# Kernel optimization log

Hardware: AMD Instinct MI355X
Metric: run time of the kernel (lower is better)

Reference implementation:

```python
import jax, jax.numpy as jnp
import numpy as np

IMG_SIZE = 224
ALPHA = 100.0  # hardcoded softmax temperature in knnsearch_t_grad


def _sqdist(a, b):
    # (B,N,C),(B,M,C) -> (B,N,M) squared euclidean distances
    return (jnp.sum(a * a, -1)[:, :, None]
            - 2.0 * jnp.einsum('bnc,bmc->bnm', a, b)
            + jnp.sum(b * b, -1)[:, None, :])


def _cdist(a, b):
    return jnp.sqrt(jnp.maximum(_sqdist(a, b), 1e-12))


def proj2img(pc, img_offset):
    # faithful jax port of GraphDeformLoss_Neural_Partial.proj2img
    B, N, _ = pc.shape
    pc_max = pc.max(axis=1)              # (B,3)
    pc_min_full = pc.min(axis=1)         # (B,3)
    pc_range = pc_max - pc_min_full
    grid_size = pc_range[:, :2].max(axis=-1) / (IMG_SIZE - 3)   # (B,)
    pc_min = pc_min_full[:, None, :2]                            # (B,1,2)
    gs = grid_size[:, None, None]
    idx_xy = jnp.floor((pc[:, :, :2] - pc_min) / gs)             # (B,N,2)
    # densify each point into a 5x5 neighborhood of pixels
    idx_dense = (idx_xy[:, :, None, :] + img_offset[None, None]).reshape(B, N * 25, 2) + 1.0
    center = jnp.floor((idx_dense.max(axis=1) + idx_dense.min(axis=1)) / 2.0)  # (B,2)
    offset = IMG_SIZE / 2.0 - center - 1.0                       # (B,2) = (offset_x, offset_y)
    idx_off = idx_dense + offset[:, None, :]
    # boundary correction as in the torch code, plus clip for safety
    idx_off = idx_off + (idx_off < 0).astype(jnp.float32) - (idx_off > IMG_SIZE - 1).astype(jnp.float32)
    idx_off = jnp.clip(idx_off, 0, IMG_SIZE - 1)
    f_dense = jnp.repeat(jnp.repeat(pc[:, :, None, 2:3], 25, axis=2).reshape(B, N * 25, 1), 3, axis=-1)
    flat = (idx_off[..., 0] * IMG_SIZE + idx_off[..., 1]).astype(jnp.int32)   # (B,N*25)
    out = jax.vmap(lambda f, i: jax.ops.segment_sum(f, i, num_segments=IMG_SIZE * IMG_SIZE))(f_dense, flat)
    img = out.reshape(B, IMG_SIZE, IMG_SIZE, 3).transpose(0, 3, 1, 2)  # (B,3,H,W)
    return jax.nn.sigmoid(img)


def setup_inputs() -> dict:
    key = jax.random.key(0)
    k1, k2, k3, k4 = jax.random.split(key, 4)
    B, N, M, C = 4, 4995, 4995, 128
    off = jnp.array([[i, j] for i in range(-2, 3) for j in range(-2, 3)], dtype=jnp.float32)
    return {
        'verts1': jax.random.normal(k1, (B, N, 3), jnp.float32),
        'verts2': jax.random.normal(k2, (B, M, 3), jnp.float32),
        'feat1': jax.random.normal(k3, (B, N, C), jnp.float32),
        'feat2': jax.random.normal(k4, (B, M, C), jnp.float32),
        'img_offset': off,
        'k': 10,
    }


def reference(verts1, verts2, feat1, feat2, img_offset, k):
    # knnsearch_t_grad: soft correspondence from feature-space cdist + softmax
    d_feat = _cdist(feat1, feat2)                               # (B,N,M)
    Pi_12 = jax.nn.softmax(-ALPHA * d_feat, axis=-1)
    verts12 = jnp.einsum('bnm,bmc->bnc', Pi_12, verts2)         # pulled-back points (B,N,3)
    # chamfer (squared distances, as chamfer_3DDist); partial: take dist1 branch (N<=M)
    d2 = _sqdist(verts12, verts2)
    self_rec_loss = jnp.mean(jnp.min(d2, axis=-1))
    # knn_grad + index_points: gather k-NN features on source cloud
    d2_11 = _sqdist(verts1, verts1)
    _, idx11 = jax.lax.top_k(-d2_11, k)                         # (B,N,k) nearest
    feat1_conv = jax.vmap(lambda p, i: p[i])(feat1, idx11)      # (B,N,k,C)
    deform_feat_loss = jnp.mean((feat1_conv - feat1[:, :, None, :]) ** 2)
    # point-to-image projection loss
    img1 = proj2img(verts12, img_offset)
    img2 = proj2img(verts2, img_offset)
    img_loss = jnp.mean((img1 - img2) ** 2)
    return self_rec_loss + img_loss + deform_feat_loss
```

## Files before the change

### kernel.cpp

```cpp
#include <hip/hip_runtime.h>
#include <math.h>

#define BB 4
#define NN 4995
#define CC 128
#define IMG 224
#define IMGP (IMG*IMG)
#define ALPHA_F 100.0f
#define SPLITS 8
#define COLS_PER_SPLIT 640
#define RBLK 40
#define NG 158
#define NCP 5120
#define NTAP (2*BB*NN*25)
#define NREP 4
#define TKCAP 256

#define SM_SCALE 20813.6898f
#define NEG2S   -41627.3796f
#define EPS_S    2.08136898e-8f

#define OFF_V12    0
#define OFF_FN1    60000
#define OFF_V1Q    81000
#define OFF_V2Q    161000
#define OFF_C2Q    241000
#define OFF_PART   323000
#define OFF_IMG1   1123000
#define OFF_IMG2   1323704
#define OFF_ACC    1524408
#define OFF_STATS  1524792
#define OFF_F2H    1525000
#define OFF_F2L    2820000
#define OFF_IMGR   4115000
#define WS_NEED_REP ((size_t)5721000*sizeof(float))
#define ZERO_START OFF_IMG1
#define ZERO_FLOATS (1524920 - OFF_IMG1)

typedef short v8s  __attribute__((ext_vector_type(8)));
typedef float v16f __attribute__((ext_vector_type(16)));

#if __has_builtin(__builtin_amdgcn_exp2f)
__device__ __forceinline__ float fast_exp2(float x){ return __builtin_amdgcn_exp2f(x); }
#else
__device__ __forceinline__ float fast_exp2(float x){ float r; asm("v_exp_f32 %0, %1" : "=v"(r) : "v"(x)); return r; }
#endif
#if __has_builtin(__builtin_amdgcn_sqrtf)
__device__ __forceinline__ float fast_sqrt(float x){ return __builtin_amdgcn_sqrtf(x); }
#else
__device__ __forceinline__ float fast_sqrt(float x){ float r; asm("v_sqrt_f32 %0, %1" : "=v"(r) : "v"(x)); return r; }
#endif

__device__ __forceinline__ float wave_min(float v){
#pragma unroll
  for (int off=32; off; off>>=1) v = fminf(v, __shfl_xor(v, off));
  return v;
}
__device__ __forceinline__ float wave_sum(float v){
#pragma unroll
  for (int off=32; off; off>>=1) v += __shfl_xor(v, off);
  return v;
}

__device__ __forceinline__ int pack_bf_hi(float a, float b){
  return (int)__builtin_amdgcn_perm(__float_as_uint(b), __float_as_uint(a), 0x07060302u);
}

__device__ __forceinline__ void cvt_hilo(float4 a, float4 c, int4& hi, int4& lo){
  float hx=__uint_as_float(__float_as_uint(a.x)&0xffff0000u);
  float hy=__uint_as_float(__float_as_uint(a.y)&0xffff0000u);
  float hz=__uint_as_float(__float_as_uint(a.z)&0xffff0000u);
  float hw=__uint_as_float(__float_as_uint(a.w)&0xffff0000u);
  float gx=__uint_as_float(__float_as_uint(c.x)&0xffff0000u);
  float gy=__uint_as_float(__float_as_uint(c.y)&0xffff0000u);
  float gz=__uint_as_float(__float_as_uint(c.z)&0xffff0000u);
  float gw=__uint_as_float(__float_as_uint(c.w)&0xffff0000u);
  hi = make_int4(pack_bf_hi(a.x,a.y), pack_bf_hi(a.z,a.w),
                 pack_bf_hi(c.x,c.y), pack_bf_hi(c.z,c.w));
  lo = make_int4(pack_bf_hi(a.x-hx,a.y-hy), pack_bf_hi(a.z-hz,a.w-hw),
                 pack_bf_hi(c.x-gx,c.y-gy), pack_bf_hi(c.z-gz,c.w-gw));
}

__device__ __forceinline__ v8s i4_to_s8(int4 v){
  union { int4 i; v8s s; } u; u.i = v; return u.s;
}

__device__ __forceinline__ void gld_lds16(const void* g, void* l){
  __builtin_amdgcn_global_load_lds((const __attribute__((address_space(1))) void*)g,
                                   (__attribute__((address_space(3))) void*)l, 16, 0, 0);
}

__device__ __forceinline__ unsigned int fkey(float f){
  unsigned int u = __float_as_uint(f);
  return ((int)u < 0) ? ~u : (u ^ 0x80000000u);
}

__global__ __launch_bounds__(256) void k_norms(const float* __restrict__ verts1, const float* __restrict__ verts2,
                        const float* __restrict__ feat1, float* __restrict__ ws) {
  int gt = blockIdx.x*blockDim.x + threadIdx.x;
  int i = gt >> 2, sub = gt & 3;
  if (i >= BB*NCP) return;
  int b = i / NCP, col = i - b*NCP;
  if (col >= NN){
    if (sub == 0)
      ((float4*)(ws+OFF_C2Q))[i] = make_float4(0.f,0.f,0.f,1e30f);
    return;
  }
  int r = b*NN + col;
  const float4* fa = (const float4*)(feat1 + (size_t)r*CC) + sub*8;
  float s1=0.f;
#pragma unroll
  for (int k=0;k<8;k++){
    float4 t = fa[k];
    s1 = fmaf(t.x,t.x,s1); s1 = fmaf(t.y,t.y,s1); s1 = fmaf(t.z,t.z,s1); s1 = fmaf(t.w,t.w,s1);
  }
  s1 += __shfl_xor(s1,1); s1 += __shfl_xor(s1,2);
  if (sub == 0){
    float x=verts1[(size_t)r*3], y=verts1[(size_t)r*3+1], z=verts1[(size_t)r*3+2];
    ((float4*)(ws+OFF_V1Q))[r] = make_float4(x,y,z, x*x+y*y+z*z);
    float x2=verts2[(size_t)r*3], y2=verts2[(size_t)r*3+1], z2=verts2[(size_t)r*3+2];
    ((float4*)(ws+OFF_V2Q))[r] = make_float4(x2,y2,z2, x2*x2+y2*y2+z2*z2);
    ws[OFF_FN1+r] = SM_SCALE*s1;
  }
}

__global__ __launch_bounds__(256) void k_conv(const float* __restrict__ feat2,
                                              const float* __restrict__ verts2,
                                              float* __restrict__ ws) {
  __shared__ float s2p[8][32];
  int g = blockIdx.x, b = blockIdx.y;
  int t = threadIdx.x;
  int q = t >> 5, c32 = t & 31;
  int col = g*32 + c32; if (col > NN-1) col = NN-1;
  const float4* src = (const float4*)(feat2 + ((size_t)(b*NN + col))*CC) + q*4;
  float4 v0 = src[0], v1 = src[1], v2 = src[2], v3 = src[3];
  {
    float s2 = 0.f;
    s2=fmaf(v0.x,v0.x,s2); s2=fmaf(v0.y,v0.y,s2); s2=fmaf(v0.z,v0.z,s2); s2=fmaf(v0.w,v0.w,s2);
    s2=fmaf(v1.x,v1.x,s2); s2=fmaf(v1.y,v1.y,s2); s2=fmaf(v1.z,v1.z,s2); s2=fmaf(v1.w,v1.w,s2);
    s2=fmaf(v2.x,v2.x,s2); s2=fmaf(v2.y,v2.y,s2); s2=fmaf(v2.z,v2.z,s2); s2=fmaf(v2.w,v2.w,s2);
    s2=fmaf(v3.x,v3.x,s2); s2=fmaf(v3.y,v3.y,s2); s2=fmaf(v3.z,v3.z,s2); s2=fmaf(v3.w,v3.w,s2);
    s2p[q][c32] = s2;
  }
  short* f2h = (short*)(ws + OFF_F2H);
  short* f2l = (short*)(ws + OFF_F2L);
  size_t base = ((size_t)(b*NG + g))*4096 + (size_t)q*512 + c32*8;
  int4 hi, lo;
  cvt_hilo(v0, v1, hi, lo);
  *(int4*)&f2h[base] = hi;  *(int4*)&f2l[base] = lo;
  cvt_hilo(v2, v3, hi, lo);
  *(int4*)&f2h[base + 256] = hi;  *(int4*)&f2l[base + 256] = lo;
  __syncthreads();
  if (t < 32){
    int c = g*32 + t;
    if (c < NN){
      float S2 = ((s2p[0][t]+s2p[1][t])+(s2p[2][t]+s2p[3][t]))
               + ((s2p[4][t]+s2p[5][t])+(s2p[6][t]+s2p[7][t]));
      size_t r = (size_t)(b*NN + c);
      float x2=verts2[r*3], y2=verts2[r*3+1], z2=verts2[r*3+2];
      ((float4*)(ws+OFF_C2Q))[(size_t)b*NCP + c] = make_float4(x2,y2,z2, SM_SCALE*S2);
    }
  }
}

__global__ __launch_bounds__(256) void k_stageA(const float* __restrict__ feat1,
      float* __restrict__ ws) {
  __shared__ __align__(16) short Bbuf[2][4096];
  __shared__ __align__(16) float colq[768*4];

  int rblk  = blockIdx.x;
  int split = blockIdx.y;
  int b     = blockIdx.z;
  int rowBase = rblk*128;
  int colBase = split*COLS_PER_SPLIT;
  int colEnd  = colBase + COLS_PER_SPLIT; if (colEnd > NN) colEnd = NN;
  int nct = (colEnd - colBase + 63) >> 6;
  int nst = nct << 2;

  int t    = threadIdx.x;
  int w    = t >> 6;
  int lane = t & 63;
  int half = lane >> 5;
  int m32  = lane & 31;

  const float* f1b = feat1 + (size_t)b*NN*CC;
  const short* f2h = (const short*)(ws + OFF_F2H);
  const short* f2l = (const short*)(ws + OFF_F2L);
  const float4* cqb = (const float4*)(ws + OFF_C2Q) + (size_t)b*NCP;

#pragma unroll
  for (int r=0; r<3; r++){
    int col = colBase + r*256 + t; if (col > NCP-1) col = NCP-1;
    gld_lds16(cqb + col, &colq[(r*256 + w*64)*4]);
  }

  size_t f2base = (((size_t)(b*NG) + (colBase>>5) + (w>>1)) << 12) + (size_t)((t&127)*8);

  {
    short* d = &Bbuf[0][0] + w*512;
    gld_lds16(f2h + f2base, d);
    gld_lds16(f2l + f2base, d + 2048);
  }

  int nrow = rowBase + w*32 + m32;
  int nclamp = nrow > NN-1 ? NN-1 : nrow;
  float sn = ws[OFF_FN1 + (size_t)b*NN + nclamp];
  const float4* ar = (const float4*)(f1b + (size_t)nclamp*CC) + (half<<1);
  v8s Afh[8], Afl[8];
#pragma unroll
  for (int sl=0; sl<8; ++sl){
    float4 v0 = ar[sl*4], v1 = ar[sl*4+1];
    int4 hi, lo;
    cvt_hilo(v0, v1, hi, lo);
    Afh[sl] = i4_to_s8(hi); Afl[sl] = i4_to_s8(lo);
  }

  __syncthreads();

  float mm = INFINITY, S = 0.f, Vx = 0.f, Vy = 0.f, Vz = 0.f;

  for (int ci = 0; ci < nct; ci++){
    v16f acc0, acc1;
#pragma unroll
    for (int i=0;i<16;i++){ acc0[i]=0.f; acc1[i]=0.f; }

#pragma unroll
    for (int kt = 0; kt < 4; kt++){
      int s = (ci<<2) + kt;
      if (s+1 < nst){
        int s1 = s+1;
        size_t so = f2base + ((size_t)(s1>>2)<<13) + ((size_t)(s1&3)<<10);
        short* d = &Bbuf[0][0] + ((s1&1)<<12) + w*512;
        gld_lds16(f2h + so, d);
        gld_lds16(f2l + so, d + 2048);
      }
      const short* Bh = &Bbuf[0][0] + ((s&1)<<12);
      const short* Bl = Bh + 2048;
#pragma unroll
      for (int kh=0; kh<2; kh++){
        int fo = (kh<<9) + (half<<8) + (m32<<3);
        v8s a0h = *(const v8s*)&Bh[fo];
        v8s a0l = *(const v8s*)&Bl[fo];
        v8s a1h = *(const v8s*)&Bh[1024+fo];
        v8s a1l = *(const v8s*)&Bl[1024+fo];
        v8s b1h = Afh[kt*2+kh];
        v8s b1l = Afl[kt*2+kh];
        __builtin_amdgcn_s_setprio(1);
        acc0 = __builtin_amdgcn_mfma_f32_32x32x16_bf16(a0h, b1h, acc0, 0,0,0);
        acc0 = __builtin_amdgcn_mfma_f32_32x32x16_bf16(a0h, b1l, acc0, 0,0,0);
        acc0 = __builtin_amdgcn_mfma_f32_32x32x16_bf16(a0l, b1h, acc0, 0,0,0);
        acc1 = __builtin_amdgcn_mfma_f32_32x32x16_bf16(a1h, b1h, acc1, 0,0,0);
        acc1 = __builtin_amdgcn_mfma_f32_32x32x16_bf16(a1h, b1l, acc1, 0,0,0);
        acc1 = __builtin_amdgcn_mfma_f32_32x32x16_bf16(a1l, b1h, acc1, 0,0,0);
        __builtin_amdgcn_s_setprio(0);
      }
      __syncthreads();
    }

    int cb4 = ci<<8;
    float Mt = INFINITY;
#pragma unroll
    for (int reg=0; reg<16; reg++){
      int cp0 = (reg&3) + 8*(reg>>2) + 4*half;
      float f0 = colq[cb4 + cp0*4 + 3];
      float d0 = fmaf(NEG2S, acc0[reg], sn) + f0;
      float p0 = fast_sqrt(fmaxf(d0, EPS_S));
      acc0[reg] = p0; Mt = fminf(Mt, p0);
      float f1v = colq[cb4 + (cp0+32)*4 + 3];
      float d1 = fmaf(NEG2S, acc1[reg], sn) + f1v;
      float p1 = fast_sqrt(fmaxf(d1, EPS_S));
      acc1[reg] = p1; Mt = fminf(Mt, p1);
    }
    float mn = fminf(mm, Mt);
    float sc = fast_exp2(mn - mm);
    float se=0.f, sx=0.f, sy=0.f, sz=0.f;
#pragma unroll
    for (int reg=0; reg<16; reg++){
      int cp0 = (reg&3) + 8*(reg>>2) + 4*half;
      float4 q0 = *(const float4*)&colq[cb4 + cp0*4];
      float e0 = fast_exp2(mn - acc0[reg]);
      se += e0; sx=fmaf(e0,q0.x,sx); sy=fmaf(e0,q0.y,sy); sz=fmaf(e0,q0.z,sz);
      float4 q1 = *(const float4*)&colq[cb4 + (cp0+32)*4];
      float e1 = fast_exp2(mn - acc1[reg]);
      se += e1; sx=fmaf(e1,q1.x,sx); sy=fmaf(e1,q1.y,sy); sz=fmaf(e1,q1.z,sz);
    }
    S  = fmaf(S,  sc, se);
    Vx = fmaf(Vx, sc, sx);
    Vy = fmaf(Vy, sc, sy);
    Vz = fmaf(Vz, sc, sz);
    mm = mn;
  }

  {
    float m2  = __shfl_xor(mm, 32);
    float S2  = __shfl_xor(S,  32);
    float Vx2 = __shfl_xor(Vx, 32);
    float Vy2 = __shfl_xor(Vy, 32);
    float Vz2 = __shfl_xor(Vz, 32);
    float M = fminf(mm, m2);
    float c1 = fast_exp2(M - mm), c2 = fast_exp2(M - m2);
    float Sf  = S*c1  + S2*c2;
    float Vxf = Vx*c1 + Vx2*c2;
    float Vyf = Vy*c1 + Vy2*c2;
    float Vzf = Vz*c1 + Vz2*c2;
    if (half==0 && nrow < NN){
      float* p = ws + OFF_PART + ((size_t)(b*NN+nrow)*SPLITS + split)*5;
      p[0]=M; p[1]=Sf; p[2]=Vxf; p[3]=Vyf; p[4]=Vzf;
    }
  }
}

__global__ void k_combine(float* __restrict__ ws) {
  int row = blockIdx.x*blockDim.x + threadIdx.x;
  if (row >= BB*NN) return;
  const float* p = ws + OFF_PART + (size_t)row*SPLITS*5;
  float mm = INFINITY;
#pragma unroll
  for (int s=0;s<SPLITS;s++) mm = fminf(mm, p[s*5]);
  float S=0.f,Vx=0.f,Vy=0.f,Vz=0.f;
#pragma unroll
  for (int s=0;s<SPLITS;s++){
    float sc = fast_exp2(mm - p[s*5]);
    S  += p[s*5+1]*sc; Vx += p[s*5+2]*sc; Vy += p[s*5+3]*sc; Vz += p[s*5+4]*sc;
  }
  ws[OFF_V12+(size_t)row*3+0]=Vx/S;
  ws[OFF_V12+(size_t)row*3+1]=Vy/S;
  ws[OFF_V12+(size_t)row*3+2]=Vz/S;
}

__global__ __launch_bounds__(256) void k_selfrec(float* __restrict__ ws) {
  int rblk = blockIdx.x, b = blockIdx.y;
  int lane = threadIdx.x & 63, w = threadIdx.x >> 6;
  int r0 = rblk*32 + w*8;
  const float4* v2q = (const float4*)(ws + OFF_V2Q) + (size_t)b*NN;
  const float* v12 = ws + OFF_V12 + (size_t)b*NN*3;
  float xr[8], yr[8], zr[8], sar[8]; bool val[8];
#pragma unroll
  for (int j=0;j<8;j++){
    int n = r0+j; val[j] = (n < NN); int nc = val[j] ? n : NN-1;
    float x=v12[(size_t)nc*3], y=v12[(size_t)nc*3+1], z=v12[(size_t)nc*3+2];
    sar[j]=x*x+y*y+z*z;
    xr[j]=-2.0f*x; yr[j]=-2.0f*y; zr[j]=-2.0f*z;
  }
  float mn[8];
#pragma unroll
  for (int j=0;j<8;j++) mn[j] = INFINITY;
  for (int m=lane; m<NN; m+=64) {
    float4 q = v2q[m];
#pragma unroll
    for (int j=0;j<8;j++)
      mn[j] = fminf(mn[j], fmaf(xr[j],q.x, fmaf(yr[j],q.y, fmaf(zr[j],q.z, q.w))));
  }
  float s = 0.f;
#pragma unroll
  for (int j=0;j<8;j++){
    float v = wave_min(mn[j]);
    s += val[j] ? (v + sar[j]) : 0.f;
  }
  if (lane==0)
    atomicAdd(((double*)(ws+OFF_ACC)) + ((rblk*4 + w) & 63), (double)s);
}

__global__ __launch_bounds__(256) void k_topk(const float* __restrict__ feat1,
        const int* __restrict__ kptr, float* __restrict__ ws) {
  __shared__ unsigned int keybuf[4*256];
  __shared__ unsigned long long cand[4*TKCAP];
  __shared__ int scnt[4];
  __shared__ float tfs[4];
  __shared__ int sel[4][16];
  __shared__ float rs[4];
  int t = threadIdx.x;
  int lane = t & 63, wid = t >> 6;
  int b = blockIdx.y;
  int n0 = blockIdx.x*4;
  int kk = *kptr; if (kk > 16) kk = 16; if (kk < 1) kk = 1;

  const float4* v1q = (const float4*)(ws + OFF_V1Q) + (size_t)b*NN;
  float mx[4], my2[4], mz[4];
#pragma unroll
  for (int j=0;j<4;j++){
    int n = n0+j; if (n > NN-1) n = NN-1;
    float4 me = v1q[n];
    mx[j]=-2.0f*me.x; my2[j]=-2.0f*me.y; mz[j]=-2.0f*me.z;
  }
  if (t < 4) scnt[t] = 0;

  float mn[4] = {INFINITY, INFINITY, INFINITY, INFINITY};
  for (int i=0;i<20;i++){
    int m = t + 256*i;
    if (m < NN){
      float4 q = v1q[m];
#pragma unroll
      for (int j=0;j<4;j++){
        float d = fmaf(mx[j], q.x, fmaf(my2[j], q.y, fmaf(mz[j], q.z, q.w)));
        mn[j] = fminf(mn[j], d);
      }
    }
  }

#pragma unroll
  for (int j=0;j<4;j++)
    keybuf[j*256 + t] = fkey(mn[j]) >> 16;
  __syncthreads();

  {
    unsigned int k0 = keybuf[wid*256 + lane];
    unsigned int k1 = keybuf[wid*256 + 64 + lane];
    unsigned int k2 = keybuf[wid*256 + 128 + lane];
    unsigned int k3 = keybuf[wid*256 + 192 + lane];
    unsigned int prefix = 0;
    for (int bit=15; bit>=0; --bit){
      unsigned int piv = prefix | (1u<<bit);
      int c = __popcll(__ballot(k0 < piv)) + __popcll(__ballot(k1 < piv))
            + __popcll(__ballot(k2 < piv)) + __popcll(__ballot(k3 < piv));
      if (c < kk) prefix = piv;
    }
    unsigned int K = (prefix<<16) | 0xFFFFu;
    unsigned int fb = (K & 0x80000000u) ? (K ^ 0x80000000u) : ~K;
    if (lane==0) tfs[wid] = __uint_as_float(fb);
  }
  __syncthreads();
  float tf0 = tfs[0], tf1 = tfs[1], tf2 = tfs[2], tf3 = tfs[3];

  bool g0 = (mn[0] <= tf0), g1 = (mn[1] <= tf1), g2 = (mn[2] <= tf2), g3 = (mn[3] <= tf3);
  if (g0|g1|g2|g3){
    for (int i=0;i<20;i++){
      int m = t + 256*i;
      if (m < NN){
        float4 q = v1q[m];
        float sw = q.w;
        float d0 = fmaf(mx[0], q.x, fmaf(my2[0], q.y, fmaf(mz[0], q.z, sw)));
        float d1 = fmaf(mx[1], q.x, fmaf(my2[1], q.y, fmaf(mz[1], q.z, sw)));
        float d2 = fmaf(mx[2], q.x, fmaf(my2[2], q.y, fmaf(mz[2], q.z, sw)));
        float d3 = fmaf(mx[3], q.x, fmaf(my2[3], q.y, fmaf(mz[3], q.z, sw)));
        if (g0 && d0 <= tf0){
          int pos = atomicAdd(&scnt[0], 1);
          if (pos < TKCAP) cand[0*TKCAP + pos] = ((unsigned long long)fkey(d0) << 13) | (unsigned int)m;
        }
        if (g1 && d1 <= tf1){
          int pos = atomicAdd(&scnt[1], 1);
          if (pos < TKCAP) cand[1*TKCAP + pos] = ((unsigned long long)fkey(d1) << 13) | (unsigned int)m;
        }
        if (g2 && d2 <= tf2){
          int pos = atomicAdd(&scnt[2], 1);
          if (pos < TKCAP) cand[2*TKCAP + pos] = ((unsigned long long)fkey(d2) << 13) | (unsigned int)m;
        }
        if (g3 && d3 <= tf3){
          int pos = atomicAdd(&scnt[3], 1);
          if (pos < TKCAP) cand[3*TKCAP + pos] = ((unsigned long long)fkey(d3) << 13) | (unsigned int)m;
        }
      }
    }
  }
  __syncthreads();

  {
    int cnt = scnt[wid]; if (cnt > TKCAP) cnt = TKCAP;
    unsigned long long kv0 = (lane       < cnt) ? cand[wid*TKCAP + lane]       : ~0ull;
    unsigned long long kv1 = (lane + 64  < cnt) ? cand[wid*TKCAP + lane + 64]  : ~0ull;
    unsigned long long kv2 = (lane + 128 < cnt) ? cand[wid*TKCAP + lane + 128] : ~0ull;
    unsigned long long kv3 = (lane + 192 < cnt) ? cand[wid*TKCAP + lane + 192] : ~0ull;
    int r0=0, r1=0, r2=0, r3=0;
    for (int q2=0; q2<cnt; ++q2){
      unsigned long long cj = cand[wid*TKCAP + q2];
      r0 += (cj < kv0); r1 += (cj < kv1); r2 += (cj < kv2); r3 += (cj < kv3);
    }
    if (lane       < cnt && r0 < kk) sel[wid][r0] = (int)(kv0 & 8191ull);
    if (lane + 64  < cnt && r1 < kk) sel[wid][r1] = (int)(kv1 & 8191ull);
    if (lane + 128 < cnt && r2 < kk) sel[wid][r2] = (int)(kv2 & 8191ull);
    if (lane + 192 < cnt && r3 < kk) sel[wid][r3] = (int)(kv3 & 8191ull);
  }
  __syncthreads();

  float mse = 0.f;
  int c = t & 127;
  int rh = t >> 7;
  for (int j=0;j<4;j++){
    int n = n0+j;
    if (n >= NN) break;
    const float* f1n = feat1 + ((size_t)b*NN + n)*CC;
    float e = f1n[c];
    for (int r=rh; r<kk; r+=2){
      const float* g = feat1 + ((size_t)b*NN + sel[j][r])*CC;
      float d = g[c]-e;
      mse = fmaf(d,d,mse);
    }
  }

  float acc = wave_sum(mse);
  if (lane==0) rs[wid] = acc;
  __syncthreads();
  if (t==0){
    float s = (rs[0]+rs[1])+(rs[2]+rs[3]);
    atomicAdd(((double*)(ws+OFF_ACC)) + 128 + ((blockIdx.x + b) & 63), (double)s);
  }
}

__global__ void k_imgstats(const float* __restrict__ verts2, const float* __restrict__ imgoff,
                           float* __restrict__ ws) {
  __shared__ float r0[4], r1[4], r2[4], r3[4];
  __shared__ float sgs, smnx, smny;
  int img = blockIdx.x >> 2, b = blockIdx.x & 3;
  const float* pc = (img==0) ? (ws + OFF_V12 + (size_t)b*NN*3) : (verts2 + (size_t)b*NN*3);
  int lane = threadIdx.x & 63, wid = threadIdx.x >> 6;
  float mnx=INFINITY, mxx=-INFINITY, mny=INFINITY, mxy=-INFINITY;
  for (int n = threadIdx.x; n < NN; n += 256) {
    float x = pc[(size_t)n*3], y = pc[(size_t)n*3+1];
    mnx=fminf(mnx,x); mxx=fmaxf(mxx,x); mny=fminf(mny,y); mxy=fmaxf(mxy,y);
  }
#pragma unroll
  for (int off=32; off; off>>=1) {
    mnx=fminf(mnx,__shfl_xor(mnx,off)); mxx=fmaxf(mxx,__shfl_xor(mxx,off));
    mny=fminf(mny,__shfl_xor(mny,off)); mxy=fmaxf(mxy,__shfl_xor(mxy,off));
  }
  if (lane==0){ r0[wid]=mnx; r1[wid]=mxx; r2[wid]=mny; r3[wid]=mxy; }
  __syncthreads();
  float* st = ws + OFF_STATS + (size_t)(img*4+b)*16;
  if (threadIdx.x==0){
    mnx=fminf(fminf(r0[0],r0[1]),fminf(r0[2],r0[3]));
    mxx=fmaxf(fmaxf(r1[0],r1[1]),fmaxf(r1[2],r1[3]));
    mny=fminf(fminf(r2[0],r2[1]),fminf(r2[2],r2[3]));
    mxy=fmaxf(fmaxf(r3[0],r3[1]),fmaxf(r3[2],r3[3]));
    float gs = fmaxf(mxx-mnx, mxy-mny) / 221.0f;
    sgs=gs; smnx=mnx; smny=mny;
    st[0]=mnx; st[1]=mxx; st[2]=mny; st[3]=mxy; st[4]=gs;
  }
  __syncthreads();
  float gs=sgs, bx=smnx, by=smny;
  float fmnx=INFINITY, fmxx=-INFINITY, fmny=INFINITY, fmxy=-INFINITY;
  for (int n = threadIdx.x; n < NN; n += 256) {
    float fx = floorf((pc[(size_t)n*3]-bx)/gs);
    float fy = floorf((pc[(size_t)n*3+1]-by)/gs);
    fmnx=fminf(fmnx,fx); fmxx=fmaxf(fmxx,fx); fmny=fminf(fmny,fy); fmxy=fmaxf(fmxy,fy);
  }
#pragma unroll
  for (int off=32; off; off>>=1) {
    fmnx=fminf(fmnx,__shfl_xor(fmnx,off)); fmxx=fmaxf(fmxx,__shfl_xor(fmxx,off));
    fmny=fminf(fmny,__shfl_xor(fmny,off)); fmxy=fmaxf(fmxy,__shfl_xor(fmxy,off));
  }
  __syncthreads();
  if (lane==0){ r0[wid]=fmnx; r1[wid]=fmxx; r2[wid]=fmny; r3[wid]=fmxy; }
  __syncthreads();
  if (threadIdx.x==0){
    fmnx=fminf(fminf(r0[0],r0[1]),fminf(r0[2],r0[3]));
    fmxx=fmaxf(fmaxf(r1[0],r1[1]),fmaxf(r1[2],r1[3]));
    fmny=fminf(fminf(r2[0],r2[1]),fminf(r2[2],r2[3]));
    fmxy=fmaxf(fmaxf(r3[0],r3[1]),fmaxf(r3[2],r3[3]));
    float omnx=INFINITY, omxx=-INFINITY, omny=INFINITY, omxy=-INFINITY;
    for (int l=0;l<25;l++){
      float ox=imgoff[l*2], oy=imgoff[l*2+1];
      omnx=fminf(omnx,ox); omxx=fmaxf(omxx,ox); omny=fminf(omny,oy); omxy=fmaxf(omxy,oy);
    }
    float cx = floorf(((fmxx+omxx+1.0f)+(fmnx+omnx+1.0f))*0.5f);
    float cy = floorf(((fmxy+omxy+1.0f)+(fmny+omny+1.0f))*0.5f);
    st[5] = (112.0f - cx) - 1.0f;
    st[6] = (112.0f - cy) - 1.0f;
  }
}

__global__ __launch_bounds__(256) void k_scatter(const float* __restrict__ verts2,
                          const float* __restrict__ imgoff,
                          float* __restrict__ ws, int nrep) {
  int g = blockIdx.x*256 + threadIdx.x;
  if (g >= NTAP) return;
  int p = g / 25; int l = g - p*25;
  int img = p / (BB*NN); int r = p - img*(BB*NN); int b = r / NN;
  const float* pc = (img==0) ? (ws + OFF_V12) : verts2;
  float x = pc[(size_t)r*3], y = pc[(size_t)r*3+1], z = pc[(size_t)r*3+2];
  const float* st = ws + OFF_STATS + (size_t)(img*4+b)*16;
  float mnx=st[0], mny=st[2], gs=st[4], offx=st[5], offy=st[6];
  float bx = floorf((x-mnx)/gs) + 1.0f + offx;
  float by = floorf((y-mny)/gs) + 1.0f + offy;
  float vx = bx + imgoff[l*2], vy = by + imgoff[l*2+1];
  vx += (vx<0.f?1.f:0.f) - (vx>223.f?1.f:0.f);
  vy += (vy<0.f?1.f:0.f) - (vy>223.f?1.f:0.f);
  vx = fminf(fmaxf(vx,0.f),223.f); vy = fminf(fmaxf(vy,0.f),223.f);
  int flat = (int)(vx*224.f + vy);
  float* im;
  if (nrep > 1)
    im = ws + OFF_IMGR + ((size_t)(((blockIdx.x & (nrep-1))*2 + img)*BB + b))*IMGP;
  else
    im = ws + (img==0?OFF_IMG1:OFF_IMG2) + (size_t)b*IMGP;
  atomicAdd(im + flat, z);
}

__global__ void k_imgloss(float* __restrict__ ws, int nrep) {
  int i = blockIdx.x*blockDim.x + threadIdx.x;
  float v = 0.f;
  if (i < BB*IMGP) {
    float a, c;
    if (nrep > 1){
      a = 0.f; c = 0.f;
      for (int r=0; r<nrep; ++r){
        a += ws[OFF_IMGR + (size_t)(r*2+0)*BB*IMGP + i];
        c += ws[OFF_IMGR + (size_t)(r*2+1)*BB*IMGP + i];
      }
    } else {
      a = ws[OFF_IMG1+i]; c = ws[OFF_IMG2+i];
    }
    float sa = 1.f/(1.f+expf(-a)), sc = 1.f/(1.f+expf(-c));
    float d = sa - sc; v = d*d;
  }
  v = wave_sum(v);
  if ((threadIdx.x&63)==0)
    atomicAdd(((double*)(ws+OFF_ACC)) + 64 + (blockIdx.x & 63), (double)v);
}

__global__ void k_final(const int* __restrict__ kptr, const float* __restrict__ ws, float* __restrict__ out) {
  const double* acc = (const double*)(ws+OFF_ACC);
  int t = threadIdx.x;
  double a0 = acc[t], a1 = acc[64+t], a2 = acc[128+t];
#pragma unroll
  for (int off=32; off; off>>=1){
    a0 += __shfl_down(a0, off);
    a1 += __shfl_down(a1, off);
    a2 += __shfl_down(a2, off);
  }
  if (t==0){
    int kk = *kptr; if (kk > 16) kk = 16; if (kk < 1) kk = 1;
    double srl = a0 / (double)(BB*NN);
    double img = a1 / ((double)BB*IMGP);
    double df  = a2 / ((double)BB*NN*kk*CC);
    out[0] = (float)(srl + img + df);
  }
}

extern "C" void kernel_launch(void* const* d_in, const int* in_sizes, int n_in,
                              void* d_out, int out_size, void* d_ws, size_t ws_size,
                              hipStream_t stream) {
  (void)in_sizes; (void)n_in; (void)out_size;
  const float* verts1 = (const float*)d_in[0];
  const float* verts2 = (const float*)d_in[1];
  const float* feat1  = (const float*)d_in[2];
  const float* feat2  = (const float*)d_in[3];
  const float* imgoff = (const float*)d_in[4];
  const int*   kptr   = (const int*)d_in[5];
  float* ws  = (float*)d_ws;
  float* out = (float*)d_out;
  int nrep = (ws_size >= WS_NEED_REP) ? NREP : 1;

  hipMemsetAsync(ws + ZERO_START, 0, (size_t)ZERO_FLOATS*sizeof(float), stream);
  if (nrep > 1)
    hipMemsetAsync(ws + OFF_IMGR, 0, (size_t)NREP*2*BB*IMGP*sizeof(float), stream);

  k_norms<<<(BB*NCP*4+255)/256, 256, 0, stream>>>(verts1, verts2, feat1, ws);

  dim3 gC(NG, BB);
  k_conv<<<gC, 256, 0, stream>>>(feat2, verts2, ws);

  dim3 gA(RBLK, SPLITS, BB);
  k_stageA<<<gA, 256, 0, stream>>>(feat1, ws);
  k_combine<<<(BB*NN+255)/256, 256, 0, stream>>>(ws);

  dim3 gS((NN+31)/32, BB);
  k_selfrec<<<gS, 256, 0, stream>>>(ws);

  dim3 gT((NN+3)/4, BB);
  k_topk<<<gT, 256, 0, stream>>>(feat1, kptr, ws);

  k_imgstats<<<8, 256, 0, stream>>>(verts2, imgoff, ws);
  k_scatter<<<(NTAP+255)/256, 256, 0, stream>>>(verts2, imgoff, ws, nrep);
  k_imgloss<<<(BB*IMGP+255)/256, 256, 0, stream>>>(ws, nrep);

  k_final<<<1,64,0,stream>>>(kptr, ws, out);
}
```

Before: 343.1 us.

## Fuse norm/convert kernels, persistent stageA with atomic work queue, merge combine into selfrec

```diff
diff --git a/kernel.cpp b/kernel.cpp
--- a/kernel.cpp
+++ b/kernel.cpp
@@ -11,10 +11,13 @@
 #define COLS_PER_SPLIT 640
 #define RBLK 40
 #define NG 158
+#define NGP 160
 #define NCP 5120
 #define NTAP (2*BB*NN*25)
 #define NREP 4
 #define TKCAP 256
+#define NITEMS (RBLK*SPLITS*BB)
+#define GRID_A 1024
 
 #define SM_SCALE 20813.6898f
 #define NEG2S   -41627.3796f
@@ -30,12 +33,14 @@
 #define OFF_IMG2   1323704
 #define OFF_ACC    1524408
 #define OFF_STATS  1524792
+#define OFF_WORK   1524920
 #define OFF_F2H    1525000
 #define OFF_F2L    2820000
 #define OFF_IMGR   4115000
 #define WS_NEED_REP ((size_t)5721000*sizeof(float))
 #define ZERO_START OFF_IMG1
-#define ZERO_FLOATS (1524920 - OFF_IMG1)
+#define ZERO_FLOATS (1524924 - OFF_IMG1)
+#define ZERO2_FLOATS (1524924 - OFF_ACC)
 
 typedef short v8s  __attribute__((ext_vector_type(8)));
 typedef float v16f __attribute__((ext_vector_type(16)));
@@ -95,41 +100,22 @@
   return ((int)u < 0) ? ~u : (u ^ 0x80000000u);
 }
 
-__global__ __launch_bounds__(256) void k_norms(const float* __restrict__ verts1, const float* __restrict__ verts2,
-                        const float* __restrict__ feat1, float* __restrict__ ws) {
-  int gt = blockIdx.x*blockDim.x + threadIdx.x;
-  int i = gt >> 2, sub = gt & 3;
-  if (i >= BB*NCP) return;
-  int b = i / NCP, col = i - b*NCP;
-  if (col >= NN){
-    if (sub == 0)
-      ((float4*)(ws+OFF_C2Q))[i] = make_float4(0.f,0.f,0.f,1e30f);
-    return;
-  }
-  int r = b*NN + col;
-  const float4* fa = (const float4*)(feat1 + (size_t)r*CC) + sub*8;
-  float s1=0.f;
-#pragma unroll
-  for (int k=0;k<8;k++){
-    float4 t = fa[k];
-    s1 = fmaf(t.x,t.x,s1); s1 = fmaf(t.y,t.y,s1); s1 = fmaf(t.z,t.z,s1); s1 = fmaf(t.w,t.w,s1);
-  }
-  s1 += __shfl_xor(s1,1); s1 += __shfl_xor(s1,2);
-  if (sub == 0){
-    float x=verts1[(size_t)r*3], y=verts1[(size_t)r*3+1], z=verts1[(size_t)r*3+2];
-    ((float4*)(ws+OFF_V1Q))[r] = make_float4(x,y,z, x*x+y*y+z*z);
-    float x2=verts2[(size_t)r*3], y2=verts2[(size_t)r*3+1], z2=verts2[(size_t)r*3+2];
-    ((float4*)(ws+OFF_V2Q))[r] = make_float4(x2,y2,z2, x2*x2+y2*y2+z2*z2);
-    ws[OFF_FN1+r] = SM_SCALE*s1;
-  }
-}
-
-__global__ __launch_bounds__(256) void k_conv(const float* __restrict__ feat2,
+__global__ __launch_bounds__(256) void k_conv(const float* __restrict__ feat1,
+                                              const float* __restrict__ feat2,
+                                              const float* __restrict__ verts1,
                                               const float* __restrict__ verts2,
                                               float* __restrict__ ws) {
-  __shared__ float s2p[8][32];
+  __shared__ float s2p[8][32], s1p[8][32];
   int g = blockIdx.x, b = blockIdx.y;
   int t = threadIdx.x;
+  if (g >= NG){
+    if (t < 32){
+      int c = g*32 + t;
+      if (c < NCP)
+        ((float4*)(ws+OFF_C2Q))[(size_t)b*NCP + c] = make_float4(0.f,0.f,0.f,1e30f);
+    }
+    return;
+  }
   int q = t >> 5, c32 = t & 31;
   int col = g*32 + c32; if (col > NN-1) col = NN-1;
   const float4* src = (const float4*)(feat2 + ((size_t)(b*NN + col))*CC) + q*4;
@@ -142,6 +128,16 @@
     s2=fmaf(v3.x,v3.x,s2); s2=fmaf(v3.y,v3.y,s2); s2=fmaf(v3.z,v3.z,s2); s2=fmaf(v3.w,v3.w,s2);
     s2p[q][c32] = s2;
   }
+  {
+    const float4* fa = (const float4*)(feat1 + ((size_t)(b*NN + col))*CC) + q*4;
+    float4 u0 = fa[0], u1 = fa[1], u2 = fa[2], u3 = fa[3];
+    float s1 = 0.f;
+    s1=fmaf(u0.x,u0.x,s1); s1=fmaf(u0.y,u0.y,s1); s1=fmaf(u0.z,u0.z,s1); s1=fmaf(u0.w,u0.w,s1);
+    s1=fmaf(u1.x,u1.x,s1); s1=fmaf(u1.y,u1.y,s1); s1=fmaf(u1.z,u1.z,s1); s1=fmaf(u1.w,u1.w,s1);
+    s1=fmaf(u2.x,u2.x,s1); s1=fmaf(u2.y,u2.y,s1); s1=fmaf(u2.z,u2.z,s1); s1=fmaf(u2.w,u2.w,s1);
+    s1=fmaf(u3.x,u3.x,s1); s1=fmaf(u3.y,u3.y,s1); s1=fmaf(u3.z,u3.z,s1); s1=fmaf(u3.w,u3.w,s1);
+    s1p[q][c32] = s1;
+  }
   short* f2h = (short*)(ws + OFF_F2H);
   short* f2l = (short*)(ws + OFF_F2L);
   size_t base = ((size_t)(b*NG + g))*4096 + (size_t)q*512 + c32*8;
@@ -156,26 +152,26 @@
     if (c < NN){
       float S2 = ((s2p[0][t]+s2p[1][t])+(s2p[2][t]+s2p[3][t]))
                + ((s2p[4][t]+s2p[5][t])+(s2p[6][t]+s2p[7][t]));
+      float S1 = ((s1p[0][t]+s1p[1][t])+(s1p[2][t]+s1p[3][t]))
+               + ((s1p[4][t]+s1p[5][t])+(s1p[6][t]+s1p[7][t]));
       size_t r = (size_t)(b*NN + c);
+      float x=verts1[r*3], y=verts1[r*3+1], z=verts1[r*3+2];
+      ((float4*)(ws+OFF_V1Q))[r] = make_float4(x,y,z, x*x+y*y+z*z);
       float x2=verts2[r*3], y2=verts2[r*3+1], z2=verts2[r*3+2];
+      ((float4*)(ws+OFF_V2Q))[r] = make_float4(x2,y2,z2, x2*x2+y2*y2+z2*z2);
       ((float4*)(ws+OFF_C2Q))[(size_t)b*NCP + c] = make_float4(x2,y2,z2, SM_SCALE*S2);
-    }
-  }
-}
-
-__global__ __launch_bounds__(256) void k_stageA(const float* __restrict__ feat1,
+      ws[OFF_FN1+r] = SM_SCALE*S1;
+    } else if (c < NCP){
+      ((float4*)(ws+OFF_C2Q))[(size_t)b*NCP + c] = make_float4(0.f,0.f,0.f,1e30f);
+    }
+  }
+}
+
+__global__ __launch_bounds__(256, 4) void k_stageA(const float* __restrict__ feat1,
       float* __restrict__ ws) {
   __shared__ __align__(16) short Bbuf[2][4096];
   __shared__ __align__(16) float colq[768*4];
-
-  int rblk  = blockIdx.x;
-  int split = blockIdx.y;
-  int b     = blockIdx.z;
-  int rowBase = rblk*128;
-  int colBase = split*COLS_PER_SPLIT;
-  int colEnd  = colBase + COLS_PER_SPLIT; if (colEnd > NN) colEnd = NN;
-  int nct = (colEnd - colBase + 63) >> 6;
-  int nst = nct << 2;
+  __shared__ int sWi;
 
   int t    = threadIdx.x;
   int w    = t >> 6;
@@ -183,162 +179,192 @@
   int half = lane >> 5;
   int m32  = lane & 31;
 
-  const float* f1b = feat1 + (size_t)b*NN*CC;
-  const short* f2h = (const short*)(ws + OFF_F2H);
-  const short* f2l = (const short*)(ws + OFF_F2L);
-  const float4* cqb = (const float4*)(ws + OFF_C2Q) + (size_t)b*NCP;
-
-#pragma unroll
-  for (int r=0; r<3; r++){
-    int col = colBase + r*256 + t; if (col > NCP-1) col = NCP-1;
-    gld_lds16(cqb + col, &colq[(r*256 + w*64)*4]);
-  }
-
-  size_t f2base = (((size_t)(b*NG) + (colBase>>5) + (w>>1)) << 12) + (size_t)((t&127)*8);
-
-  {
-    short* d = &Bbuf[0][0] + w*512;
-    gld_lds16(f2h + f2base, d);
-    gld_lds16(f2l + f2base, d + 2048);
-  }
-
-  int nrow = rowBase + w*32 + m32;
-  int nclamp = nrow > NN-1 ? NN-1 : nrow;
-  float sn = ws[OFF_FN1 + (size_t)b*NN + nclamp];
-  const float4* ar = (const float4*)(f1b + (size_t)nclamp*CC) + (half<<1);
-  v8s Afh[8], Afl[8];
-#pragma unroll
-  for (int sl=0; sl<8; ++sl){
-    float4 v0 = ar[sl*4], v1 = ar[sl*4+1];
-    int4 hi, lo;
-    cvt_hilo(v0, v1, hi, lo);
-    Afh[sl] = i4_to_s8(hi); Afl[sl] = i4_to_s8(lo);
-  }
-
-  __syncthreads();
-
-  float mm = INFINITY, S = 0.f, Vx = 0.f, Vy = 0.f, Vz = 0.f;
-
-  for (int ci = 0; ci < nct; ci++){
-    v16f acc0, acc1;
-#pragma unroll
-    for (int i=0;i<16;i++){ acc0[i]=0.f; acc1[i]=0.f; }
-
-#pragma unroll
-    for (int kt = 0; kt < 4; kt++){
-      int s = (ci<<2) + kt;
-      if (s+1 < nst){
-        int s1 = s+1;
-        size_t so = f2base + ((size_t)(s1>>2)<<13) + ((size_t)(s1&3)<<10);
-        short* d = &Bbuf[0][0] + ((s1&1)<<12) + w*512;
-        gld_lds16(f2h + so, d);
-        gld_lds16(f2l + so, d + 2048);
+  int* wcnt = (int*)(ws + OFF_WORK);
+  if (t == 0) sWi = atomicAdd(wcnt, 1);
+  __syncthreads();
+
+  while (sWi < NITEMS) {
+    int wi = sWi;
+    int rblk  = wi % RBLK;
+    int qd    = wi / RBLK;
+    int split = qd & 7;
+    int b     = qd >> 3;
+    int rowBase = rblk*128;
+    int colBase = split*COLS_PER_SPLIT;
+    int colEnd  = colBase + COLS_PER_SPLIT; if (colEnd > NN) colEnd = NN;
+    int nct = (colEnd - colBase + 63) >> 6;
+    int nst = nct << 2;
+
+    const float* f1b = feat1 + (size_t)b*NN*CC;
+    const short* f2h = (const short*)(ws + OFF_F2H);
+    const short* f2l = (const short*)(ws + OFF_F2L);
+    const float4* cqb = (const float4*)(ws + OFF_C2Q) + (size_t)b*NCP;
+
+#pragma unroll
+    for (int r=0; r<3; r++){
+      int col = colBase + r*256 + t; if (col > NCP-1) col = NCP-1;
+      gld_lds16(cqb + col, &colq[(r*256 + w*64)*4]);
+    }
+
+    size_t f2base = (((size_t)(b*NG) + (colBase>>5) + (w>>1)) << 12) + (size_t)((t&127)*8);
+
+    {
+      short* d = &Bbuf[0][0] + w*512;
+      gld_lds16(f2h + f2base, d);
+      gld_lds16(f2l + f2base, d + 2048);
+    }
+
+    int nrow = rowBase + w*32 + m32;
+    int nclamp = nrow > NN-1 ? NN-1 : nrow;
+    float sn = ws[OFF_FN1 + (size_t)b*NN + nclamp];
+    const float4* ar = (const float4*)(f1b + (size_t)nclamp*CC) + (half<<1);
+    v8s Afh[8], Afl[8];
+#pragma unroll
+    for (int sl=0; sl<8; ++sl){
+      float4 v0 = ar[sl*4], v1 = ar[sl*4+1];
+      int4 hi, lo;
+      cvt_hilo(v0, v1, hi, lo);
+      Afh[sl] = i4_to_s8(hi); Afl[sl] = i4_to_s8(lo);
+    }
+
+    __syncthreads();
+
+    float mm = INFINITY, S = 0.f, Vx = 0.f, Vy = 0.f, Vz = 0.f;
+
+    for (int ci = 0; ci < nct; ci++){
+      v16f acc0, acc1;
+#pragma unroll
+      for (int i=0;i<16;i++){ acc0[i]=0.f; acc1[i]=0.f; }
+
+#pragma unroll
+      for (int kt = 0; kt < 4; kt++){
+        int s = (ci<<2) + kt;
+        if (s+1 < nst){
+          int s1 = s+1;
+          size_t so = f2base + ((size_t)(s1>>2)<<13) + ((size_t)(s1&3)<<10);
+          short* d = &Bbuf[0][0] + ((s1&1)<<12) + w*512;
+          gld_lds16(f2h + so, d);
+          gld_lds16(f2l + so, d + 2048);
+        }
+        const short* Bh = &Bbuf[0][0] + ((s&1)<<12);
+        const short* Bl = Bh + 2048;
+#pragma unroll
+        for (int kh=0; kh<2; kh++){
+          int fo = (kh<<9) + (half<<8) + (m32<<3);
+          v8s a0h = *(const v8s*)&Bh[fo];
+          v8s a0l = *(const v8s*)&Bl[fo];
+          v8s a1h = *(const v8s*)&Bh[1024+fo];
+          v8s a1l = *(const v8s*)&Bl[1024+fo];
+          v8s b1h = Afh[kt*2+kh];
+          v8s b1l = Afl[kt*2+kh];
+          __builtin_amdgcn_s_setprio(1);
+          acc0 = __builtin_amdgcn_mfma_f32_32x32x16_bf16(a0h, b1h, acc0, 0,0,0);
+          acc0 = __builtin_amdgcn_mfma_f32_32x32x16_bf16(a0h, b1l, acc0, 0,0,0);
+          acc0 = __builtin_amdgcn_mfma_f32_32x32x16_bf16(a0l, b1h, acc0, 0,0,0);
+          acc1 = __builtin_amdgcn_mfma_f32_32x32x16_bf16(a1h, b1h, acc1, 0,0,0);
+          acc1 = __builtin_amdgcn_mfma_f32_32x32x16_bf16(a1h, b1l, acc1, 0,0,0);
+          acc1 = __builtin_amdgcn_mfma_f32_32x32x16_bf16(a1l, b1h, acc1, 0,0,0);
+          __builtin_amdgcn_s_setprio(0);
+        }
+        __syncthreads();
       }
-      const short* Bh = &Bbuf[0][0] + ((s&1)<<12);
-      const short* Bl = Bh + 2048;
-#pragma unroll
-      for (int kh=0; kh<2; kh++){
-        int fo = (kh<<9) + (half<<8) + (m32<<3);
-        v8s a0h = *(const v8s*)&Bh[fo];
-        v8s a0l = *(const v8s*)&Bl[fo];
-        v8s a1h = *(const v8s*)&Bh[1024+fo];
-        v8s a1l = *(const v8s*)&Bl[1024+fo];
-        v8s b1h = Afh[kt*2+kh];
-        v8s b1l = Afl[kt*2+kh];
-        __builtin_amdgcn_s_setprio(1);
-        acc0 = __builtin_amdgcn_mfma_f32_32x32x16_bf16(a0h, b1h, acc0, 0,0,0);
-        acc0 = __builtin_amdgcn_mfma_f32_32x32x16_bf16(a0h, b1l, acc0, 0,0,0);
-        acc0 = __builtin_amdgcn_mfma_f32_32x32x16_bf16(a0l, b1h, acc0, 0,0,0);
-        acc1 = __builtin_amdgcn_mfma_f32_32x32x16_bf16(a1h, b1h, acc1, 0,0,0);
-        acc1 = __builtin_amdgcn_mfma_f32_32x32x16_bf16(a1h, b1l, acc1, 0,0,0);
-        acc1 = __builtin_amdgcn_mfma_f32_32x32x16_bf16(a1l, b1h, acc1, 0,0,0);
-        __builtin_amdgcn_s_setprio(0);
+
+      int cb4 = ci<<8;
+      float Mt = INFINITY;
+#pragma unroll
+      for (int reg=0; reg<16; reg++){
+        int cp0 = (reg&3) + 8*(reg>>2) + 4*half;
+        float f0 = colq[cb4 + cp0*4 + 3];
+        float d0 = fmaf(NEG2S, acc0[reg], sn) + f0;
+        float p0 = fast_sqrt(fmaxf(d0, EPS_S));
+        acc0[reg] = p0; Mt = fminf(Mt, p0);
+        float f1v = colq[cb4 + (cp0+32)*4 + 3];
+        float d1 = fmaf(NEG2S, acc1[reg], sn) + f1v;
+        float p1 = fast_sqrt(fmaxf(d1, EPS_S));
+        acc1[reg] = p1; Mt = fminf(Mt, p1);
       }
-      __syncthreads();
-    }
-
-    int cb4 = ci<<8;
-    float Mt = INFINITY;
-#pragma unroll
-    for (int reg=0; reg<16; reg++){
-      int cp0 = (reg&3) + 8*(reg>>2) + 4*half;
-      float f0 = colq[cb4 + cp0*4 + 3];
-      float d0 = fmaf(NEG2S, acc0[reg], sn) + f0;
-      float p0 = fast_sqrt(fmaxf(d0, EPS_S));
-      acc0[reg] = p0; Mt = fminf(Mt, p0);
-      float f1v = colq[cb4 + (cp0+32)*4 + 3];
-      float d1 = fmaf(NEG2S, acc1[reg], sn) + f1v;
-      float p1 = fast_sqrt(fmaxf(d1, EPS_S));
-      acc1[reg] = p1; Mt = fminf(Mt, p1);
-    }
-    float mn = fminf(mm, Mt);
-    float sc = fast_exp2(mn - mm);
-    float se=0.f, sx=0.f, sy=0.f, sz=0.f;
-#pragma unroll
-    for (int reg=0; reg<16; reg++){
-      int cp0 = (reg&3) + 8*(reg>>2) + 4*half;
-      float4 q0 = *(const float4*)&colq[cb4 + cp0*4];
-      float e0 = fast_exp2(mn - acc0[reg]);
-      se += e0; sx=fmaf(e0,q0.x,sx); sy=fmaf(e0,q0.y,sy); sz=fmaf(e0,q0.z,sz);
-      float4 q1 = *(const float4*)&colq[cb4 + (cp0+32)*4];
-      float e1 = fast_exp2(mn - acc1[reg]);
-      se += e1; sx=fmaf(e1,q1.x,sx); sy=fmaf(e1,q1.y,sy); sz=fmaf(e1,q1.z,sz);
-    }
-    S  = fmaf(S,  sc, se);
-    Vx = fmaf(Vx, sc, sx);
-    Vy = fmaf(Vy, sc, sy);
-    Vz = fmaf(Vz, sc, sz);
-    mm = mn;
-  }
-
-  {
-    float m2  = __shfl_xor(mm, 32);
-    float S2  = __shfl_xor(S,  32);
-    float Vx2 = __shfl_xor(Vx, 32);
-    float Vy2 = __shfl_xor(Vy, 32);
-    float Vz2 = __shfl_xor(Vz, 32);
-    float M = fminf(mm, m2);
-    float c1 = fast_exp2(M - mm), c2 = fast_exp2(M - m2);
-    float Sf  = S*c1  + S2*c2;
-    float Vxf = Vx*c1 + Vx2*c2;
-    float Vyf = Vy*c1 + Vy2*c2;
-    float Vzf = Vz*c1 + Vz2*c2;
-    if (half==0 && nrow < NN){
-      float* p = ws + OFF_PART + ((size_t)(b*NN+nrow)*SPLITS + split)*5;
-      p[0]=M; p[1]=Sf; p[2]=Vxf; p[3]=Vyf; p[4]=Vzf;
-    }
-  }
-}
-
-__global__ void k_combine(float* __restrict__ ws) {
-  int row = blockIdx.x*blockDim.x + threadIdx.x;
-  if (row >= BB*NN) return;
-  const float* p = ws + OFF_PART + (size_t)row*SPLITS*5;
-  float mm = INFINITY;
-#pragma unroll
-  for (int s=0;s<SPLITS;s++) mm = fminf(mm, p[s*5]);
-  float S=0.f,Vx=0.f,Vy=0.f,Vz=0.f;
-#pragma unroll
-  for (int s=0;s<SPLITS;s++){
-    float sc = fast_exp2(mm - p[s*5]);
-    S  += p[s*5+1]*sc; Vx += p[s*5+2]*sc; Vy += p[s*5+3]*sc; Vz += p[s*5+4]*sc;
-  }
-  ws[OFF_V12+(size_t)row*3+0]=Vx/S;
-  ws[OFF_V12+(size_t)row*3+1]=Vy/S;
-  ws[OFF_V12+(size_t)row*3+2]=Vz/S;
+      float mn = fminf(mm, Mt);
+      float sc = fast_exp2(mn - mm);
+      float se=0.f, sx=0.f, sy=0.f, sz=0.f;
+#pragma unroll
+      for (int reg=0; reg<16; reg++){
+        int cp0 = (reg&3) + 8*(reg>>2) + 4*half;
+        float4 q0 = *(const float4*)&colq[cb4 + cp0*4];
+        float e0 = fast_exp2(mn - acc0[reg]);
+        se += e0; sx=fmaf(e0,q0.x,sx); sy=fmaf(e0,q0.y,sy); sz=fmaf(e0,q0.z,sz);
+        float4 q1 = *(const float4*)&colq[cb4 + (cp0+32)*4];
+        float e1 = fast_exp2(mn - acc1[reg]);
+        se += e1; sx=fmaf(e1,q1.x,sx); sy=fmaf(e1,q1.y,sy); sz=fmaf(e1,q1.z,sz);
+      }
+      S  = fmaf(S,  sc, se);
+      Vx = fmaf(Vx, sc, sx);
+      Vy = fmaf(Vy, sc, sy);
+      Vz = fmaf(Vz, sc, sz);
+      mm = mn;
+    }
+
+    {
+      float m2  = __shfl_xor(mm, 32);
+      float S2  = __shfl_xor(S,  32);
+      float Vx2 = __shfl_xor(Vx, 32);
+      float Vy2 = __shfl_xor(Vy, 32);
+      float Vz2 = __shfl_xor(Vz, 32);
+      float M = fminf(mm, m2);
+      float c1 = fast_exp2(M - mm), c2 = fast_exp2(M - m2);
+      float Sf  = S*c1  + S2*c2;
+      float Vxf = Vx*c1 + Vx2*c2;
+      float Vyf = Vy*c1 + Vy2*c2;
+      float Vzf = Vz*c1 + Vz2*c2;
+      if (half==0 && nrow < NN){
+        float* p = ws + OFF_PART + ((size_t)(b*NN+nrow)*SPLITS + split)*5;
+        p[0]=M; p[1]=Sf; p[2]=Vxf; p[3]=Vyf; p[4]=Vzf;
+      }
+    }
+
+    __syncthreads();
+    if (t == 0) sWi = atomicAdd(wcnt, 1);
+    __syncthreads();
+  }
 }
 
 __global__ __launch_bounds__(256) void k_selfrec(float* __restrict__ ws) {
+  __shared__ float v12s[32][3];
   int rblk = blockIdx.x, b = blockIdx.y;
-  int lane = threadIdx.x & 63, w = threadIdx.x >> 6;
-  int r0 = rblk*32 + w*8;
+  int t = threadIdx.x;
+  int lane = t & 63, w = t >> 6;
+  int r0blk = rblk*32;
+
+  if (t < 32){
+    int row = r0blk + t;
+    int rowc = row > NN-1 ? NN-1 : row;
+    const float* p = ws + OFF_PART + (size_t)(b*NN+rowc)*SPLITS*5;
+    float mm = INFINITY;
+#pragma unroll
+    for (int s=0;s<SPLITS;s++) mm = fminf(mm, p[s*5]);
+    float S=0.f,Vx=0.f,Vy=0.f,Vz=0.f;
+#pragma unroll
+    for (int s=0;s<SPLITS;s++){
+      float sc = fast_exp2(mm - p[s*5]);
+      S  += p[s*5+1]*sc; Vx += p[s*5+2]*sc; Vy += p[s*5+3]*sc; Vz += p[s*5+4]*sc;
+    }
+    float ox = Vx/S, oy = Vy/S, oz = Vz/S;
+    v12s[t][0]=ox; v12s[t][1]=oy; v12s[t][2]=oz;
+    if (row < NN){
+      ws[OFF_V12+(size_t)(b*NN+row)*3+0]=ox;
+      ws[OFF_V12+(size_t)(b*NN+row)*3+1]=oy;
+      ws[OFF_V12+(size_t)(b*NN+row)*3+2]=oz;
+    }
+  }
+  __syncthreads();
+
+  int r0 = r0blk + w*8;
   const float4* v2q = (const float4*)(ws + OFF_V2Q) + (size_t)b*NN;
-  const float* v12 = ws + OFF_V12 + (size_t)b*NN*3;
   float xr[8], yr[8], zr[8], sar[8]; bool val[8];
 #pragma unroll
   for (int j=0;j<8;j++){
-    int n = r0+j; val[j] = (n < NN); int nc = val[j] ? n : NN-1;
-    float x=v12[(size_t)nc*3], y=v12[(size_t)nc*3+1], z=v12[(size_t)nc*3+2];
+    int n = r0+j; val[j] = (n < NN);
+    int li = w*8+j;
+    float x=v12s[li][0], y=v12s[li][1], z=v12s[li][2];
     sar[j]=x*x+y*y+z*z;
     xr[j]=-2.0f*x; yr[j]=-2.0f*y; zr[j]=-2.0f*z;
   }
@@ -496,15 +522,15 @@
   }
 }
 
-__global__ void k_imgstats(const float* __restrict__ verts2, const float* __restrict__ imgoff,
+__global__ __launch_bounds__(1024) void k_imgstats(const float* __restrict__ verts2, const float* __restrict__ imgoff,
                            float* __restrict__ ws) {
-  __shared__ float r0[4], r1[4], r2[4], r3[4];
+  __shared__ float r0[16], r1[16], r2[16], r3[16];
   __shared__ float sgs, smnx, smny;
   int img = blockIdx.x >> 2, b = blockIdx.x & 3;
   const float* pc = (img==0) ? (ws + OFF_V12 + (size_t)b*NN*3) : (verts2 + (size_t)b*NN*3);
   int lane = threadIdx.x & 63, wid = threadIdx.x >> 6;
   float mnx=INFINITY, mxx=-INFINITY, mny=INFINITY, mxy=-INFINITY;
-  for (int n = threadIdx.x; n < NN; n += 256) {
+  for (int n = threadIdx.x; n < NN; n += 1024) {
     float x = pc[(size_t)n*3], y = pc[(size_t)n*3+1];
     mnx=fminf(mnx,x); mxx=fmaxf(mxx,x); mny=fminf(mny,y); mxy=fmaxf(mxy,y);
   }
@@ -517,10 +543,11 @@
   __syncthreads();
   float* st = ws + OFF_STATS + (size_t)(img*4+b)*16;
   if (threadIdx.x==0){
-    mnx=fminf(fminf(r0[0],r0[1]),fminf(r0[2],r0[3]));
-    mxx=fmaxf(fmaxf(r1[0],r1[1]),fmaxf(r1[2],r1[3]));
-    mny=fminf(fminf(r2[0],r2[1]),fminf(r2[2],r2[3]));
-    mxy=fmaxf(fmaxf(r3[0],r3[1]),fmaxf(r3[2],r3[3]));
+    mnx=r0[0]; mxx=r1[0]; mny=r2[0]; mxy=r3[0];
+    for (int i=1;i<16;i++){
+      mnx=fminf(mnx,r0[i]); mxx=fmaxf(mxx,r1[i]);
+      mny=fminf(mny,r2[i]); mxy=fmaxf(mxy,r3[i]);
+    }
     float gs = fmaxf(mxx-mnx, mxy-mny) / 221.0f;
     sgs=gs; smnx=mnx; smny=mny;
     st[0]=mnx; st[1]=mxx; st[2]=mny; st[3]=mxy; st[4]=gs;
@@ -528,7 +555,7 @@
   __syncthreads();
   float gs=sgs, bx=smnx, by=smny;
   float fmnx=INFINITY, fmxx=-INFINITY, fmny=INFINITY, fmxy=-INFINITY;
-  for (int n = threadIdx.x; n < NN; n += 256) {
+  for (int n = threadIdx.x; n < NN; n += 1024) {
     float fx = floorf((pc[(size_t)n*3]-bx)/gs);
     float fy = floorf((pc[(size_t)n*3+1]-by)/gs);
     fmnx=fminf(fmnx,fx); fmxx=fmaxf(fmxx,fx); fmny=fminf(fmny,fy); fmxy=fmaxf(fmxy,fy);
@@ -542,10 +569,11 @@
   if (lane==0){ r0[wid]=fmnx; r1[wid]=fmxx; r2[wid]=fmny; r3[wid]=fmxy; }
   __syncthreads();
   if (threadIdx.x==0){
-    fmnx=fminf(fminf(r0[0],r0[1]),fminf(r0[2],r0[3]));
-    fmxx=fmaxf(fmaxf(r1[0],r1[1]),fmaxf(r1[2],r1[3]));
-    fmny=fminf(fminf(r2[0],r2[1]),fminf(r2[2],r2[3]));
-    fmxy=fmaxf(fmaxf(r3[0],r3[1]),fmaxf(r3[2],r3[3]));
+    fmnx=r0[0]; fmxx=r1[0]; fmny=r2[0]; fmxy=r3[0];
+    for (int i=1;i<16;i++){
+      fmnx=fminf(fmnx,r0[i]); fmxx=fmaxf(fmxx,r1[i]);
+      fmny=fminf(fmny,r2[i]); fmxy=fmaxf(fmxy,r3[i]);
+    }
     float omnx=INFINITY, omxx=-INFINITY, omny=INFINITY, omxy=-INFINITY;
     for (int l=0;l<25;l++){
       float ox=imgoff[l*2], oy=imgoff[l*2+1];
@@ -639,18 +667,17 @@
   float* out = (float*)d_out;
   int nrep = (ws_size >= WS_NEED_REP) ? NREP : 1;
 
-  hipMemsetAsync(ws + ZERO_START, 0, (size_t)ZERO_FLOATS*sizeof(float), stream);
-  if (nrep > 1)
+  if (nrep > 1){
+    hipMemsetAsync(ws + OFF_ACC, 0, (size_t)ZERO2_FLOATS*sizeof(float), stream);
     hipMemsetAsync(ws + OFF_IMGR, 0, (size_t)NREP*2*BB*IMGP*sizeof(float), stream);
-
-  k_norms<<<(BB*NCP*4+255)/256, 256, 0, stream>>>(verts1, verts2, feat1, ws);
-
-  dim3 gC(NG, BB);
-  k_conv<<<gC, 256, 0, stream>>>(feat2, verts2, ws);
-
-  dim3 gA(RBLK, SPLITS, BB);
-  k_stageA<<<gA, 256, 0, stream>>>(feat1, ws);
-  k_combine<<<(BB*NN+255)/256, 256, 0, stream>>>(ws);
+  } else {
+    hipMemsetAsync(ws + ZERO_START, 0, (size_t)ZERO_FLOATS*sizeof(float), stream);
+  }
+
+  dim3 gC(NGP, BB);
+  k_conv<<<gC, 256, 0, stream>>>(feat1, feat2, verts1, verts2, ws);
+
+  k_stageA<<<GRID_A, 256, 0, stream>>>(feat1, ws);
 
   dim3 gS((NN+31)/32, BB);
   k_selfrec<<<gS, 256, 0, stream>>>(ws);
@@ -658,7 +685,7 @@
   dim3 gT((NN+3)/4, BB);
   k_topk<<<gT, 256, 0, stream>>>(feat1, kptr, ws);
 
-  k_imgstats<<<8, 256, 0, stream>>>(verts2, imgoff, ws);
+  k_imgstats<<<8, 1024, 0, stream>>>(verts2, imgoff, ws);
   k_scatter<<<(NTAP+255)/256, 256, 0, stream>>>(verts2, imgoff, ws, nrep);
   k_imgloss<<<(BB*IMGP+255)/256, 256, 0, stream>>>(ws, nrep);
 
```

Result: slower. 594.0 us (+73.1%).
